# Kernel tuning notes

Measured on AMD Instinct MI355X. Metric: run time of the kernel, lower is better.

## Reference

```python
import jax, jax.numpy as jnp
import numpy as np

H_NODE = 256
H_EDGE = 64
B = 8        # number of graphs
A_PER = 64   # anchors per graph
N_PER = 512  # nodes per graph
INF = 1000000.0
EPS = 1e-8
D_MIN, D_MAX = 0.0, 20.0  # _rbf defaults (gvp-style)


def setup_inputs() -> dict:
    key = jax.random.key(0)
    ks = jax.random.split(key, 16)
    h, he = H_NODE, H_EDGE
    n = lambda k, shp, s=1.0: jax.random.normal(k, shp, jnp.float32) * s
    return {
        "anchor_x": n(ks[0], (B * A_PER, 3), 10.0),
        "node_x": n(ks[1], (B * N_PER, 3), 10.0),
        "anchor_features": n(ks[2], (B * A_PER, h)),
        "node_features": n(ks[3], (B * N_PER, h)),
        "batch": jnp.repeat(jnp.arange(B, dtype=jnp.int32), N_PER),
        "anchor_batch": jnp.repeat(jnp.arange(B, dtype=jnp.int32), A_PER),
        "node_mask": (jax.random.uniform(ks[4], (B * N_PER,)) < 0.9).astype(jnp.float32),
        "Wq": n(ks[5], (h, h), h ** -0.5), "bq": jnp.zeros((h,), jnp.float32),
        "Wkv": n(ks[6], (2 * h, h + he), (h + he) ** -0.5), "bkv": jnp.zeros((2 * h,), jnp.float32),
        "ln1_g": jnp.ones((h,), jnp.float32), "ln1_b": jnp.zeros((h,), jnp.float32),
        "W1": n(ks[7], (2 * h, h), h ** -0.5), "b1": jnp.zeros((2 * h,), jnp.float32),
        "W2": n(ks[8], (2 * h, 2 * h), (2 * h) ** -0.5), "b2": jnp.zeros((2 * h,), jnp.float32),
        "W3": n(ks[9], (h, 2 * h), (2 * h) ** -0.5), "b3": jnp.zeros((h,), jnp.float32),
        "ln2_g": jnp.ones((h,), jnp.float32), "ln2_b": jnp.zeros((h,), jnp.float32),
    }


def _ln(x, g, b, eps=1e-5):
    m = x.mean(-1, keepdims=True)
    v = ((x - m) ** 2).mean(-1, keepdims=True)
    return (x - m) * jax.lax.rsqrt(v + eps) * g + b


def _forward(anchor_x, node_x, anchor_features, node_features, node_mask,
             Wq, bq, Wkv, bkv, ln1_g, ln1_b, W1, b1, W2, b2, W3, b3, ln2_g, ln2_b):
    h, he = H_NODE, H_EDGE
    # equal-sized graphs: reshape global tensors to [B, ., .] (batch ids are repeat(arange(B)))
    q = (anchor_features @ Wq.T + bq).reshape(B, A_PER, h)
    ax = anchor_x.reshape(B, A_PER, 3)
    nx = node_x.reshape(B, N_PER, 3)
    nf = node_features.reshape(B, N_PER, h)
    mask = node_mask.reshape(B, N_PER)

    # pairwise anchor->node distances; original adds scalar eps to the diff vector before the norm
    dist = jnp.linalg.norm(ax[:, :, None, :] - nx[:, None, :, :] + EPS, axis=-1)  # [B,A,N]

    # RBF featurization of dist/10 with D_count = h_edge
    mu = jnp.linspace(D_MIN, D_MAX, he)
    sigma = (D_MAX - D_MIN) / he
    rbf = jnp.exp(-(((dist / 10.0)[..., None] - mu) / sigma) ** 2)  # [B,A,N,he]

    # kv_node(cat([node_feat, rbf])) decomposed: node part computed once per node
    Wkv_n, Wkv_e = Wkv[:, :h], Wkv[:, h:]
    kv_n = nf @ Wkv_n.T + bkv                 # [B,N,2h]
    kv_e = rbf @ Wkv_e.T                      # [B,A,N,2h]
    kv = kv_n[:, None, :, :] + kv_e           # [B,A,N,2h]
    k, v = kv[..., :h], kv[..., h:]

    attn = jnp.einsum('bah,banh->ban', q, k)
    attn = attn * ((mask[:, None, :] - 1.0) * INF)  # faithful to original (multiplicative mask)
    attn = jax.nn.softmax(attn, axis=-1)
    upd = jnp.einsum('ban,banh->bah', attn, v).reshape(B * A_PER, h)

    af = _ln(anchor_features + upd, ln1_g, ln1_b)
    m = jax.nn.relu(af @ W1.T + b1)
    m = jax.nn.relu(m @ W2.T + b2)
    m = m @ W3.T + b3
    return _ln(af + m, ln2_g, ln2_b)


def reference(anchor_x, node_x, anchor_features, node_features, batch, anchor_batch, node_mask,
              Wq, bq, Wkv, bkv, ln1_g, ln1_b, W1, b1, W2, b2, W3, b3, ln2_g, ln2_b):
    # batch / anchor_batch encode equal-sized contiguous graphs; structure is baked into reshapes
    return _forward(anchor_x, node_x, anchor_features, node_features, node_mask,
                    Wq, bq, Wkv, bkv, ln1_g, ln1_b, W1, b1, W2, b2, W3, b3, ln2_g, ln2_b)
```

## Files before the change

kernel.cpp:

```cpp
#include <hip/hip_runtime.h>

#define H    256
#define HE   64
#define NPB  512
#define MU_STEP (20.0f / 63.0f)
#define INV_SIG 3.2f

__device__ __forceinline__ float wave_sum(float v) {
#pragma unroll
    for (int o = 32; o; o >>= 1) v += __shfl_xor(v, o, 64);
    return v;
}
__device__ __forceinline__ float wave_max(float v) {
#pragma unroll
    for (int o = 32; o; o >>= 1) v = fmaxf(v, __shfl_xor(v, o, 64));
    return v;
}
__device__ __forceinline__ float dot4(float4 a, float4 b, float acc) {
    return fmaf(a.x, b.x, fmaf(a.y, b.y, fmaf(a.z, b.z, fmaf(a.w, b.w, acc))));
}
__device__ __forceinline__ float4 add4(float4 a, float4 b) {
    return make_float4(a.x + b.x, a.y + b.y, a.z + b.z, a.w + b.w);
}

__global__ void __launch_bounds__(1024, 4) fused_all(
    const float* __restrict__ anchor_x, const float* __restrict__ node_x,
    const float* __restrict__ anchor_f, const float* __restrict__ node_f,
    const float* __restrict__ node_mask,
    const float* __restrict__ Wq,  const float* __restrict__ bq,
    const float* __restrict__ Wkv, const float* __restrict__ bkv,
    const float* __restrict__ ln1_g, const float* __restrict__ ln1_b,
    const float* __restrict__ W1, const float* __restrict__ b1,
    const float* __restrict__ W2, const float* __restrict__ b2,
    const float* __restrict__ W3, const float* __restrict__ b3,
    const float* __restrict__ g2,  const float* __restrict__ bb2,
    float* __restrict__ out)
{
    const int bid = blockIdx.x;
    const int b  = bid & 7;
    const int pr = bid >> 3;
    const int aA = b * 64 + 2 * pr;
    const int aB = aA + 1;
    const int t  = threadIdx.x;
    const int wv = t >> 6, l = t & 63;
    const int sub = l >> 4, kc16 = l & 15;

    __shared__ __align__(16) float qWp_s[2][2][324];
    __shared__ __align__(16) float q_s[2][256];
    __shared__ __align__(16) float af_s[2][256];
    __shared__ __align__(16) float d10_s[2][NPB];
    __shared__ __align__(16) float mf_s[NPB];
    __shared__ __align__(16) float lg_s[2][NPB];
    __shared__ __align__(16) float w_s[2][NPB];
    __shared__ __align__(16) float snf_s[2][256], rj_s[2][64];
    __shared__ __align__(16) float m1_s[2][512], m2_s[2][512];
    __shared__ __align__(16) float red[512], red16[32];
    __shared__ int   idx_s[2][NPB];
    __shared__ int   cnt_s[2];

    if (t < 128) {
        int hh = t >> 6, tt = t & 63;
        ((float4*)af_s[hh])[tt] =
            ((const float4*)anchor_f)[(size_t)(hh ? aB : aA) * 64 + tt];
    }
    if (t < 2) cnt_s[t] = 0;

    if (t < 512) {
        float axA0 = anchor_x[3 * aA], axA1 = anchor_x[3 * aA + 1], axA2 = anchor_x[3 * aA + 2];
        float axB0 = anchor_x[3 * aB], axB1 = anchor_x[3 * aB + 1], axB2 = anchor_x[3 * aB + 2];
        int ng = b * NPB + t;
        float nx0 = node_x[3 * ng], nx1 = node_x[3 * ng + 1], nx2 = node_x[3 * ng + 2];
        float dx = axA0 - nx0 + 1e-8f, dy = axA1 - nx1 + 1e-8f, dz = axA2 - nx2 + 1e-8f;
        d10_s[0][t] = sqrtf(dx * dx + dy * dy + dz * dz) * 0.1f;
        dx = axB0 - nx0 + 1e-8f; dy = axB1 - nx1 + 1e-8f; dz = axB2 - nx2 + 1e-8f;
        d10_s[1][t] = sqrtf(dx * dx + dy * dy + dz * dz) * 0.1f;
        mf_s[t] = (node_mask[ng] - 1.0f) * 1000000.0f;
    }
    __syncthreads();

    {
        float4 aA4[4], aB4[4];
#pragma unroll
        for (int v = 0; v < 4; ++v) {
            aA4[v] = ((const float4*)af_s[0])[16 * v + kc16];
            aB4[v] = ((const float4*)af_s[1])[16 * v + kc16];
        }
#pragma unroll
        for (int pass = 0; pass < 4; ++pass) {
            int m = pass * 64 + wv * 4 + sub;
            const float4* wr = (const float4*)(Wq + (size_t)m * 256);
            float4 w[4];
#pragma unroll
            for (int v = 0; v < 4; ++v) w[v] = wr[16 * v + kc16];
            float aAc = 0.f, aBc = 0.f;
#pragma unroll
            for (int v = 0; v < 4; ++v) {
                aAc = dot4(w[v], aA4[v], aAc);
                aBc = dot4(w[v], aB4[v], aBc);
            }
#pragma unroll
            for (int o = 8; o >= 1; o >>= 1) {
                aAc += __shfl_xor(aAc, o, 64);
                aBc += __shfl_xor(aBc, o, 64);
            }
            if (kc16 == 0) {
                float bv = bq[m];
                q_s[0][m] = aAc + bv;
                q_s[1][m] = aBc + bv;
            }
        }
    }
    __syncthreads();

    {
        int grp = -1, col = 0;
        if (t < 320)                   { grp = 0; col = t; }
        else if (t >= 512 && t < 832)  { grp = 1; col = t - 512; }
        if (grp >= 0) {
            const int r0 = grp * 128;
            const float* qsA = q_s[0] + r0;
            const float* qsB = q_s[1] + r0;
            float accA = 0.f, accB = 0.f;
            for (int o = 0; o < 128; o += 16) {
                float w16[16];
#pragma unroll
                for (int u = 0; u < 16; ++u) w16[u] = Wkv[(size_t)(r0 + o + u) * 320 + col];
#pragma unroll
                for (int u = 0; u < 16; ++u) {
                    accA = fmaf(w16[u], qsA[o + u], accA);
                    accB = fmaf(w16[u], qsB[o + u], accB);
                }
            }
            qWp_s[grp][0][col] = accA;
            qWp_s[grp][1][col] = accB;
        }
    }
    {
        float p = (t < 512) ? q_s[t >> 8][t & 255] * bkv[t & 255] : 0.f;
        p = wave_sum(p);
        if (l == 0) red16[wv] = p;
    }
    __syncthreads();
    const float qbkA = red16[0] + red16[1] + red16[2] + red16[3];
    const float qbkB = red16[4] + red16[5] + red16[6] + red16[7];

    {
        const int g = sub;
        float4 qA4[4], qB4[4];
#pragma unroll
        for (int v = 0; v < 4; ++v) {
            qA4[v] = add4(((const float4*)qWp_s[0][0])[4 * kc16 + v],
                          ((const float4*)qWp_s[1][0])[4 * kc16 + v]);
            qB4[v] = add4(((const float4*)qWp_s[0][1])[4 * kc16 + v],
                          ((const float4*)qWp_s[1][1])[4 * kc16 + v]);
        }
        const float4 qeA4 = add4(((const float4*)(qWp_s[0][0] + 256))[kc16],
                                 ((const float4*)(qWp_s[1][0] + 256))[kc16]);
        const float4 qeB4 = add4(((const float4*)(qWp_s[0][1] + 256))[kc16],
                                 ((const float4*)(qWp_s[1][1] + 256))[kc16]);
        const float mu0 = (4 * kc16 + 0) * MU_STEP, mu1 = (4 * kc16 + 1) * MU_STEP;
        const float mu2 = (4 * kc16 + 2) * MU_STEP, mu3 = (4 * kc16 + 3) * MU_STEP;
        const float4* nfb = (const float4*)(node_f + (size_t)(b * NPB) * 256);

        float4 f[4], fn[4];
        {
            const size_t r0 = (size_t)(wv * 4 + g) * 64 + 4 * kc16;
#pragma unroll
            for (int v = 0; v < 4; ++v) f[v] = nfb[r0 + v];
        }
        for (int it = 0; it < 8; ++it) {
            const int n = it * 64 + wv * 4 + g;
            if (it < 7) {
                const size_t r1 = (size_t)(n + 64) * 64 + 4 * kc16;
#pragma unroll
                for (int v = 0; v < 4; ++v) fn[v] = nfb[r1 + v];
            }
            float sA = 0.f, sB = 0.f;
#pragma unroll
            for (int v = 0; v < 4; ++v) {
                sA = dot4(f[v], qA4[v], sA);
                sB = dot4(f[v], qB4[v], sB);
            }
            const float dA10 = d10_s[0][n], dB10 = d10_s[1][n];
            float u;
            u = (dA10 - mu0) * INV_SIG; sA = fmaf(qeA4.x, __expf(-u * u), sA);
            u = (dA10 - mu1) * INV_SIG; sA = fmaf(qeA4.y, __expf(-u * u), sA);
            u = (dA10 - mu2) * INV_SIG; sA = fmaf(qeA4.z, __expf(-u * u), sA);
            u = (dA10 - mu3) * INV_SIG; sA = fmaf(qeA4.w, __expf(-u * u), sA);
            u = (dB10 - mu0) * INV_SIG; sB = fmaf(qeB4.x, __expf(-u * u), sB);
            u = (dB10 - mu1) * INV_SIG; sB = fmaf(qeB4.y, __expf(-u * u), sB);
            u = (dB10 - mu2) * INV_SIG; sB = fmaf(qeB4.z, __expf(-u * u), sB);
            u = (dB10 - mu3) * INV_SIG; sB = fmaf(qeB4.w, __expf(-u * u), sB);
#pragma unroll
            for (int o = 8; o >= 1; o >>= 1) {
                sA += __shfl_xor(sA, o, 64);
                sB += __shfl_xor(sB, o, 64);
            }
            if (kc16 == 0) {
                lg_s[0][n] = (sA + qbkA) * mf_s[n];
                lg_s[1][n] = (sB + qbkB) * mf_s[n];
            }
#pragma unroll
            for (int v = 0; v < 4; ++v) f[v] = fn[v];
        }
    }
    __syncthreads();

    const int h8 = t >> 9, n9 = t & 511;
    float lg = lg_s[h8][n9];
    {
        float m = wave_max(lg);
        if (l == 0) red16[wv] = m;
    }
    __syncthreads();
    float gmA = red16[0], gmB = red16[8];
#pragma unroll
    for (int i = 1; i < 8; ++i) { gmA = fmaxf(gmA, red16[i]); gmB = fmaxf(gmB, red16[8 + i]); }
    float e = __expf(lg - (h8 ? gmB : gmA));
    w_s[h8][n9] = e;
    {
        float sm = wave_sum(e);
        if (l == 0) red16[16 + wv] = sm;
    }
    if (e > 0.f) { int p = atomicAdd(&cnt_s[h8], 1); idx_s[h8][p] = n9; }
    __syncthreads();
    float smA = 0.f, smB = 0.f;
#pragma unroll
    for (int i = 0; i < 8; ++i) { smA += red16[16 + i]; smB += red16[24 + i]; }
    const float invA = 1.0f / smA, invB = 1.0f / smB;

    if (t < 512) {
        const int hh = t >> 8, col = t & 255;
        const int cnt = cnt_s[hh];
        const float* base = node_f + (size_t)(b * NPB) * 256 + col;
        const int*   idx  = idx_s[hh];
        const float* ws   = w_s[hh];
        float s = 0.f;
        int i = 0;
        for (; i + 16 <= cnt; i += 16) {
            int   n[16];
            float f[16];
#pragma unroll
            for (int u = 0; u < 16; ++u) n[u] = idx[i + u];
#pragma unroll
            for (int u = 0; u < 16; ++u) f[u] = base[(size_t)n[u] * 256];
#pragma unroll
            for (int u = 0; u < 16; ++u) s = fmaf(ws[n[u]], f[u], s);
        }
        for (; i < cnt; ++i) { int n = idx[i]; s = fmaf(ws[n], base[(size_t)n * 256], s); }
        snf_s[hh][col] = s;
    } else {
        const int tt = t - 512;
        const int ha = tt >> 8, j = tt & 63, g = (tt >> 6) & 3;
        const int cnt = cnt_s[ha];
        const int*   idx = idx_s[ha];
        const float* ws  = w_s[ha];
        const float* ds  = d10_s[ha];
        const float mu = j * MU_STEP;
        float r = 0.f;
        int i = g;
        for (; i + 12 < cnt; i += 16) {
            int n0 = idx[i], n1 = idx[i + 4], n2 = idx[i + 8], n3 = idx[i + 12];
            float u0 = (ds[n0] - mu) * INV_SIG, u1 = (ds[n1] - mu) * INV_SIG;
            float u2 = (ds[n2] - mu) * INV_SIG, u3 = (ds[n3] - mu) * INV_SIG;
            r = fmaf(ws[n0], __expf(-u0 * u0), r);
            r = fmaf(ws[n1], __expf(-u1 * u1), r);
            r = fmaf(ws[n2], __expf(-u2 * u2), r);
            r = fmaf(ws[n3], __expf(-u3 * u3), r);
        }
        for (; i < cnt; i += 4) {
            int n = idx[i];
            float uu = (ds[n] - mu) * INV_SIG;
            r = fmaf(ws[n], __expf(-uu * uu), r);
        }
        red[tt] = r;
    }
    __syncthreads();
    if (t < 128) {
        int ha = t >> 6, j = t & 63;
        rj_s[ha][j] = red[ha * 256 + j] + red[ha * 256 + 64 + j]
                    + red[ha * 256 + 128 + j] + red[ha * 256 + 192 + j];
    }
    __syncthreads();

    {
        float4 sA4[4], sB4[4];
#pragma unroll
        for (int v = 0; v < 4; ++v) {
            sA4[v] = ((const float4*)snf_s[0])[16 * v + kc16];
            sB4[v] = ((const float4*)snf_s[1])[16 * v + kc16];
        }
        const float4 rA4 = ((const float4*)rj_s[0])[kc16];
        const float4 rB4 = ((const float4*)rj_s[1])[kc16];
#pragma unroll
        for (int pass = 0; pass < 4; ++pass) {
            int m = pass * 64 + wv * 4 + sub;
            const float4* wr = (const float4*)(Wkv + (size_t)(256 + m) * 320);
            float4 w[4];
#pragma unroll
            for (int v = 0; v < 4; ++v) w[v] = wr[16 * v + kc16];
            float4 w4 = wr[64 + kc16];
            float aAc = 0.f, aBc = 0.f;
#pragma unroll
            for (int v = 0; v < 4; ++v) {
                aAc = dot4(w[v], sA4[v], aAc);
                aBc = dot4(w[v], sB4[v], aBc);
            }
            aAc = dot4(w4, rA4, aAc);
            aBc = dot4(w4, rB4, aBc);
#pragma unroll
            for (int o = 8; o >= 1; o >>= 1) {
                aAc += __shfl_xor(aAc, o, 64);
                aBc += __shfl_xor(aBc, o, 64);
            }
            if (kc16 == 0) { red[m] = aAc; red[256 + m] = aBc; }
        }
    }
    __syncthreads();

    const int h = (t >> 8) & 1, th = t & 255;
    float x = 0.f;
    if (t < 512)
        x = af_s[h][th] + red[h * 256 + th] * (h ? invB : invA) + bkv[256 + th];
    {
        float s1 = wave_sum(x);
        float s2 = wave_sum(x * x);
        if (l == 0) { red16[wv] = s1; red16[16 + wv] = s2; }
    }
    __syncthreads();
    {
        float meanA = (red16[0] + red16[1] + red16[2] + red16[3]) * (1.0f / 256.0f);
        float meanB = (red16[4] + red16[5] + red16[6] + red16[7]) * (1.0f / 256.0f);
        float sqA   = (red16[16] + red16[17] + red16[18] + red16[19]) * (1.0f / 256.0f);
        float sqB   = (red16[20] + red16[21] + red16[22] + red16[23]) * (1.0f / 256.0f);
        float varA = sqA - meanA * meanA, varB = sqB - meanB * meanB;
        if (t < 512) {
            float xc = x - (h ? meanB : meanA);
            af_s[h][th] = xc * rsqrtf((h ? varB : varA) + 1e-5f) * ln1_g[th] + ln1_b[th];
        }
    }
    __syncthreads();

    {
        float4 aA4[4], aB4[4];
#pragma unroll
        for (int v = 0; v < 4; ++v) {
            aA4[v] = ((const float4*)af_s[0])[16 * v + kc16];
            aB4[v] = ((const float4*)af_s[1])[16 * v + kc16];
        }
#pragma unroll
        for (int pass = 0; pass < 8; ++pass) {
            int m = pass * 64 + wv * 4 + sub;
            const float4* wr = (const float4*)(W1 + (size_t)m * 256);
            float4 w[4];
#pragma unroll
            for (int v = 0; v < 4; ++v) w[v] = wr[16 * v + kc16];
            float aAc = 0.f, aBc = 0.f;
#pragma unroll
            for (int v = 0; v < 4; ++v) {
                aAc = dot4(w[v], aA4[v], aAc);
                aBc = dot4(w[v], aB4[v], aBc);
            }
#pragma unroll
            for (int o = 8; o >= 1; o >>= 1) {
                aAc += __shfl_xor(aAc, o, 64);
                aBc += __shfl_xor(aBc, o, 64);
            }
            if (kc16 == 0) {
                float bv = b1[m];
                m1_s[0][m] = fmaxf(aAc + bv, 0.f);
                m1_s[1][m] = fmaxf(aBc + bv, 0.f);
            }
        }
    }
    __syncthreads();

#pragma unroll
    for (int pass = 0; pass < 8; ++pass) {
        int m = pass * 64 + wv * 4 + sub;
        const float4* wr = (const float4*)(W2 + (size_t)m * 512);
        float4 w[8];
#pragma unroll
        for (int k = 0; k < 8; ++k) w[k] = wr[k * 16 + kc16];
        const float4* mA = (const float4*)m1_s[0];
        const float4* mB = (const float4*)m1_s[1];
        float aAc = 0.f, aBc = 0.f;
#pragma unroll
        for (int k = 0; k < 8; ++k) {
            aAc = dot4(w[k], mA[k * 16 + kc16], aAc);
            aBc = dot4(w[k], mB[k * 16 + kc16], aBc);
        }
#pragma unroll
        for (int o = 8; o >= 1; o >>= 1) {
            aAc += __shfl_xor(aAc, o, 64);
            aBc += __shfl_xor(aBc, o, 64);
        }
        if (kc16 == 0) {
            float bv = b2[m];
            m2_s[0][m] = fmaxf(aAc + bv, 0.f);
            m2_s[1][m] = fmaxf(aBc + bv, 0.f);
        }
    }
    __syncthreads();

#pragma unroll
    for (int pass = 0; pass < 4; ++pass) {
        int m = pass * 64 + wv * 4 + sub;
        const float4* wr = (const float4*)(W3 + (size_t)m * 512);
        float4 w[8];
#pragma unroll
        for (int k = 0; k < 8; ++k) w[k] = wr[k * 16 + kc16];
        const float4* mA = (const float4*)m2_s[0];
        const float4* mB = (const float4*)m2_s[1];
        float aAc = 0.f, aBc = 0.f;
#pragma unroll
        for (int k = 0; k < 8; ++k) {
            aAc = dot4(w[k], mA[k * 16 + kc16], aAc);
            aBc = dot4(w[k], mB[k * 16 + kc16], aBc);
        }
#pragma unroll
        for (int o = 8; o >= 1; o >>= 1) {
            aAc += __shfl_xor(aAc, o, 64);
            aBc += __shfl_xor(aBc, o, 64);
        }
        if (kc16 == 0) {
            float bv = b3[m];
            red[m]       = aAc + bv;
            red[256 + m] = aBc + bv;
        }
    }
    __syncthreads();

    float y = 0.f;
    if (t < 512) y = red[h * 256 + th] + af_s[h][th];
    {
        float s1 = wave_sum(y);
        float s2 = wave_sum(y * y);
        if (l == 0) { red16[wv] = s1; red16[16 + wv] = s2; }
    }
    __syncthreads();
    {
        float mnA = (red16[0] + red16[1] + red16[2] + red16[3]) * (1.0f / 256.0f);
        float mnB = (red16[4] + red16[5] + red16[6] + red16[7]) * (1.0f / 256.0f);
        float sqA = (red16[16] + red16[17] + red16[18] + red16[19]) * (1.0f / 256.0f);
        float sqB = (red16[20] + red16[21] + red16[22] + red16[23]) * (1.0f / 256.0f);
        float vrA = sqA - mnA * mnA, vrB = sqB - mnB * mnB;
        if (t < 512) {
            float yc = y - (h ? mnB : mnA);
            int aOut = h ? aB : aA;
            out[(size_t)aOut * 256 + th] =
                yc * rsqrtf((h ? vrB : vrA) + 1e-5f) * g2[th] + bb2[th];
        }
    }
}

extern "C" void kernel_launch(void* const* d_in, const int* in_sizes, int n_in,
                              void* d_out, int out_size, void* d_ws, size_t ws_size,
                              hipStream_t stream)
{
    const float* anchor_x  = (const float*)d_in[0];
    const float* node_x    = (const float*)d_in[1];
    const float* anchor_f  = (const float*)d_in[2];
    const float* node_f    = (const float*)d_in[3];
    const float* node_mask = (const float*)d_in[6];
    const float* Wq        = (const float*)d_in[7];
    const float* bq        = (const float*)d_in[8];
    const float* Wkv       = (const float*)d_in[9];
    const float* bkv       = (const float*)d_in[10];
    const float* ln1_g     = (const float*)d_in[11];
    const float* ln1_b     = (const float*)d_in[12];
    const float* W1        = (const float*)d_in[13];
    const float* b1        = (const float*)d_in[14];
    const float* W2        = (const float*)d_in[15];
    const float* b2        = (const float*)d_in[16];
    const float* W3        = (const float*)d_in[17];
    const float* b3        = (const float*)d_in[18];
    const float* ln2_g     = (const float*)d_in[19];
    const float* ln2_b     = (const float*)d_in[20];

    fused_all<<<256, 1024, 0, stream>>>(anchor_x, node_x, anchor_f, node_f,
                                        node_mask, Wq, bq, Wkv, bkv,
                                        ln1_g, ln1_b, W1, b1, W2, b2, W3, b3,
                                        ln2_g, ln2_b, (float*)d_out);
}
```

Baseline: 144.7 us.

## Software-pipeline weight loads and replace sparse index gather with dense loops

Adds double-buffered register prefetch of weight rows across passes in the Wq, Wkv, W1, W2 and W3 matvecs, so global loads for the next pass are issued before the current pass's FMAs. It also removes the atomic compaction of nonzero softmax weights into an index list. The node-feature and RBF reductions now loop densely over all 512 nodes with prefetched loads and several independent accumulators. The aim is to hide memory latency and drop the atomic and the indirect gathers. The cost is extra register pressure and about 10% more work on masked nodes whose weight is zero.

```diff
diff --git a/kernel.cpp b/kernel.cpp
--- a/kernel.cpp
+++ b/kernel.cpp
@@ -55,15 +55,12 @@
     __shared__ __align__(16) float snf_s[2][256], rj_s[2][64];
     __shared__ __align__(16) float m1_s[2][512], m2_s[2][512];
     __shared__ __align__(16) float red[512], red16[32];
-    __shared__ int   idx_s[2][NPB];
-    __shared__ int   cnt_s[2];
 
     if (t < 128) {
         int hh = t >> 6, tt = t & 63;
         ((float4*)af_s[hh])[tt] =
             ((const float4*)anchor_f)[(size_t)(hh ? aB : aA) * 64 + tt];
     }
-    if (t < 2) cnt_s[t] = 0;
 
     if (t < 512) {
         float axA0 = anchor_x[3 * aA], axA1 = anchor_x[3 * aA + 1], axA2 = anchor_x[3 * aA + 2];
@@ -85,18 +82,26 @@
             aA4[v] = ((const float4*)af_s[0])[16 * v + kc16];
             aB4[v] = ((const float4*)af_s[1])[16 * v + kc16];
         }
+        float4 w0[4], w1[4];
+        {
+            const float4* wr = (const float4*)(Wq + (size_t)(wv * 4 + sub) * 256);
+#pragma unroll
+            for (int v = 0; v < 4; ++v) w0[v] = wr[16 * v + kc16];
+        }
 #pragma unroll
         for (int pass = 0; pass < 4; ++pass) {
-            int m = pass * 64 + wv * 4 + sub;
-            const float4* wr = (const float4*)(Wq + (size_t)m * 256);
-            float4 w[4];
-#pragma unroll
-            for (int v = 0; v < 4; ++v) w[v] = wr[16 * v + kc16];
+            float4* wc = (pass & 1) ? w1 : w0;
+            float4* wn = (pass & 1) ? w0 : w1;
+            if (pass < 3) {
+                const float4* wr = (const float4*)(Wq + (size_t)((pass + 1) * 64 + wv * 4 + sub) * 256);
+#pragma unroll
+                for (int v = 0; v < 4; ++v) wn[v] = wr[16 * v + kc16];
+            }
             float aAc = 0.f, aBc = 0.f;
 #pragma unroll
             for (int v = 0; v < 4; ++v) {
-                aAc = dot4(w[v], aA4[v], aAc);
-                aBc = dot4(w[v], aB4[v], aBc);
+                aAc = dot4(wc[v], aA4[v], aAc);
+                aBc = dot4(wc[v], aB4[v], aBc);
             }
 #pragma unroll
             for (int o = 8; o >= 1; o >>= 1) {
@@ -104,6 +109,7 @@
                 aBc += __shfl_xor(aBc, o, 64);
             }
             if (kc16 == 0) {
+                int m = pass * 64 + wv * 4 + sub;
                 float bv = bq[m];
                 q_s[0][m] = aAc + bv;
                 q_s[1][m] = aBc + bv;
@@ -121,14 +127,26 @@
             const float* qsA = q_s[0] + r0;
             const float* qsB = q_s[1] + r0;
             float accA = 0.f, accB = 0.f;
-            for (int o = 0; o < 128; o += 16) {
-                float w16[16];
-#pragma unroll
-                for (int u = 0; u < 16; ++u) w16[u] = Wkv[(size_t)(r0 + o + u) * 320 + col];
+            float wb0[16], wb1[16];
+#pragma unroll
+            for (int u = 0; u < 16; ++u) wb0[u] = Wkv[(size_t)(r0 + u) * 320 + col];
+#pragma unroll
+            for (int o = 0; o < 128; o += 32) {
+#pragma unroll
+                for (int u = 0; u < 16; ++u) wb1[u] = Wkv[(size_t)(r0 + o + 16 + u) * 320 + col];
 #pragma unroll
                 for (int u = 0; u < 16; ++u) {
-                    accA = fmaf(w16[u], qsA[o + u], accA);
-                    accB = fmaf(w16[u], qsB[o + u], accB);
+                    accA = fmaf(wb0[u], qsA[o + u], accA);
+                    accB = fmaf(wb0[u], qsB[o + u], accB);
+                }
+                if (o + 32 < 128) {
+#pragma unroll
+                    for (int u = 0; u < 16; ++u) wb0[u] = Wkv[(size_t)(r0 + o + 32 + u) * 320 + col];
+                }
+#pragma unroll
+                for (int u = 0; u < 16; ++u) {
+                    accA = fmaf(wb1[u], qsA[o + 16 + u], accA);
+                    accB = fmaf(wb1[u], qsB[o + 16 + u], accB);
                 }
             }
             qWp_s[grp][0][col] = accA;
@@ -222,7 +240,6 @@
         float sm = wave_sum(e);
         if (l == 0) red16[16 + wv] = sm;
     }
-    if (e > 0.f) { int p = atomicAdd(&cnt_s[h8], 1); idx_s[h8][p] = n9; }
     __syncthreads();
     float smA = 0.f, smB = 0.f;
 #pragma unroll
@@ -231,49 +248,43 @@
 
     if (t < 512) {
         const int hh = t >> 8, col = t & 255;
-        const int cnt = cnt_s[hh];
         const float* base = node_f + (size_t)(b * NPB) * 256 + col;
-        const int*   idx  = idx_s[hh];
         const float* ws   = w_s[hh];
         float s = 0.f;
-        int i = 0;
-        for (; i + 16 <= cnt; i += 16) {
-            int   n[16];
-            float f[16];
-#pragma unroll
-            for (int u = 0; u < 16; ++u) n[u] = idx[i + u];
-#pragma unroll
-            for (int u = 0; u < 16; ++u) f[u] = base[(size_t)n[u] * 256];
-#pragma unroll
-            for (int u = 0; u < 16; ++u) s = fmaf(ws[n[u]], f[u], s);
-        }
-        for (; i < cnt; ++i) { int n = idx[i]; s = fmaf(ws[n], base[(size_t)n * 256], s); }
+        float f0[8], f1[8];
+#pragma unroll
+        for (int u = 0; u < 8; ++u) f0[u] = base[(size_t)u * 256];
+        for (int i = 0; i < 512; i += 16) {
+#pragma unroll
+            for (int u = 0; u < 8; ++u) f1[u] = base[(size_t)(i + 8 + u) * 256];
+#pragma unroll
+            for (int u = 0; u < 8; ++u) s = fmaf(ws[i + u], f0[u], s);
+            if (i + 16 < 512) {
+#pragma unroll
+                for (int u = 0; u < 8; ++u) f0[u] = base[(size_t)(i + 16 + u) * 256];
+            }
+#pragma unroll
+            for (int u = 0; u < 8; ++u) s = fmaf(ws[i + 8 + u], f1[u], s);
+        }
         snf_s[hh][col] = s;
     } else {
         const int tt = t - 512;
-        const int ha = tt >> 8, j = tt & 63, g = (tt >> 6) & 3;
-        const int cnt = cnt_s[ha];
-        const int*   idx = idx_s[ha];
-        const float* ws  = w_s[ha];
-        const float* ds  = d10_s[ha];
+        const int ha = tt >> 8, j = tt & 63, g4 = (tt >> 6) & 3;
+        const float* ws = w_s[ha];
+        const float* ds = d10_s[ha];
         const float mu = j * MU_STEP;
-        float r = 0.f;
-        int i = g;
-        for (; i + 12 < cnt; i += 16) {
-            int n0 = idx[i], n1 = idx[i + 4], n2 = idx[i + 8], n3 = idx[i + 12];
-            float u0 = (ds[n0] - mu) * INV_SIG, u1 = (ds[n1] - mu) * INV_SIG;
-            float u2 = (ds[n2] - mu) * INV_SIG, u3 = (ds[n3] - mu) * INV_SIG;
-            r = fmaf(ws[n0], __expf(-u0 * u0), r);
-            r = fmaf(ws[n1], __expf(-u1 * u1), r);
-            r = fmaf(ws[n2], __expf(-u2 * u2), r);
-            r = fmaf(ws[n3], __expf(-u3 * u3), r);
-        }
-        for (; i < cnt; i += 4) {
-            int n = idx[i];
-            float uu = (ds[n] - mu) * INV_SIG;
-            r = fmaf(ws[n], __expf(-uu * uu), r);
-        }
-        red[tt] = r;
+        float r0 = 0.f, r1 = 0.f, r2 = 0.f, r3 = 0.f;
+        for (int i = g4; i < 512; i += 16) {
+            float u0 = (ds[i]      - mu) * INV_SIG;
+            float u1 = (ds[i + 4]  - mu) * INV_SIG;
+            float u2 = (ds[i + 8]  - mu) * INV_SIG;
+            float u3 = (ds[i + 12] - mu) * INV_SIG;
+            r0 = fmaf(ws[i],      __expf(-u0 * u0), r0);
+            r1 = fmaf(ws[i + 4],  __expf(-u1 * u1), r1);
+            r2 = fmaf(ws[i + 8],  __expf(-u2 * u2), r2);
+            r3 = fmaf(ws[i + 12], __expf(-u3 * u3), r3);
+        }
+        red[tt] = (r0 + r1) + (r2 + r3);
     }
     __syncthreads();
     if (t < 128) {
@@ -292,28 +303,41 @@
         }
         const float4 rA4 = ((const float4*)rj_s[0])[kc16];
         const float4 rB4 = ((const float4*)rj_s[1])[kc16];
+        float4 w0[4], w1[4], w40, w41;
+        {
+            const float4* wr = (const float4*)(Wkv + (size_t)(256 + wv * 4 + sub) * 320);
+#pragma unroll
+            for (int v = 0; v < 4; ++v) w0[v] = wr[16 * v + kc16];
+            w40 = wr[64 + kc16];
+        }
 #pragma unroll
         for (int pass = 0; pass < 4; ++pass) {
-            int m = pass * 64 + wv * 4 + sub;
-            const float4* wr = (const float4*)(Wkv + (size_t)(256 + m) * 320);
-            float4 w[4];
-#pragma unroll
-            for (int v = 0; v < 4; ++v) w[v] = wr[16 * v + kc16];
-            float4 w4 = wr[64 + kc16];
+            float4* wc = (pass & 1) ? w1 : w0;
+            float4* wn = (pass & 1) ? w0 : w1;
+            float4  w4c = (pass & 1) ? w41 : w40;
+            if (pass < 3) {
+                const float4* wr = (const float4*)(Wkv + (size_t)(256 + (pass + 1) * 64 + wv * 4 + sub) * 320);
+#pragma unroll
+                for (int v = 0; v < 4; ++v) wn[v] = wr[16 * v + kc16];
+                if (pass & 1) w40 = wr[64 + kc16]; else w41 = wr[64 + kc16];
+            }
             float aAc = 0.f, aBc = 0.f;
 #pragma unroll
             for (int v = 0; v < 4; ++v) {
-                aAc = dot4(w[v], sA4[v], aAc);
-                aBc = dot4(w[v], sB4[v], aBc);
-            }
-            aAc = dot4(w4, rA4, aAc);
-            aBc = dot4(w4, rB4, aBc);
+                aAc = dot4(wc[v], sA4[v], aAc);
+                aBc = dot4(wc[v], sB4[v], aBc);
+            }
+            aAc = dot4(w4c, rA4, aAc);
+            aBc = dot4(w4c, rB4, aBc);
 #pragma unroll
             for (int o = 8; o >= 1; o >>= 1) {
                 aAc += __shfl_xor(aAc, o, 64);
                 aBc += __shfl_xor(aBc, o, 64);
             }
-            if (kc16 == 0) { red[m] = aAc; red[256 + m] = aBc; }
+            if (kc16 == 0) {
+                int m = pass * 64 + wv * 4 + sub;
+                red[m] = aAc; red[256 + m] = aBc;
+            }
         }
     }
     __syncthreads();
@@ -348,18 +372,26 @@
             aA4[v] = ((const float4*)af_s[0])[16 * v + kc16];
             aB4[v] = ((const float4*)af_s[1])[16 * v + kc16];
         }
+        float4 w0[4], w1[4];
+        {
+            const float4* wr = (const float4*)(W1 + (size_t)(wv * 4 + sub) * 256);
+#pragma unroll
+            for (int v = 0; v < 4; ++v) w0[v] = wr[16 * v + kc16];
+        }
 #pragma unroll
         for (int pass = 0; pass < 8; ++pass) {
-            int m = pass * 64 + wv * 4 + sub;
-            const float4* wr = (const float4*)(W1 + (size_t)m * 256);
-            float4 w[4];
-#pragma unroll
-            for (int v = 0; v < 4; ++v) w[v] = wr[16 * v + kc16];
+            float4* wc = (pass & 1) ? w1 : w0;
+            float4* wn = (pass & 1) ? w0 : w1;
+            if (pass < 7) {
+                const float4* wr = (const float4*)(W1 + (size_t)((pass + 1) * 64 + wv * 4 + sub) * 256);
+#pragma unroll
+                for (int v = 0; v < 4; ++v) wn[v] = wr[16 * v + kc16];
+            }
             float aAc = 0.f, aBc = 0.f;
 #pragma unroll
             for (int v = 0; v < 4; ++v) {
-                aAc = dot4(w[v], aA4[v], aAc);
-                aBc = dot4(w[v], aB4[v], aBc);
+                aAc = dot4(wc[v], aA4[v], aAc);
+                aBc = dot4(wc[v], aB4[v], aBc);
             }
 #pragma unroll
             for (int o = 8; o >= 1; o >>= 1) {
@@ -367,6 +399,7 @@
                 aBc += __shfl_xor(aBc, o, 64);
             }
             if (kc16 == 0) {
+                int m = pass * 64 + wv * 4 + sub;
                 float bv = b1[m];
                 m1_s[0][m] = fmaxf(aAc + bv, 0.f);
                 m1_s[1][m] = fmaxf(aBc + bv, 0.f);
@@ -375,58 +408,92 @@
     }
     __syncthreads();
 
-#pragma unroll
-    for (int pass = 0; pass < 8; ++pass) {
-        int m = pass * 64 + wv * 4 + sub;
-        const float4* wr = (const float4*)(W2 + (size_t)m * 512);
-        float4 w[8];
-#pragma unroll
-        for (int k = 0; k < 8; ++k) w[k] = wr[k * 16 + kc16];
+    {
         const float4* mA = (const float4*)m1_s[0];
         const float4* mB = (const float4*)m1_s[1];
-        float aAc = 0.f, aBc = 0.f;
-#pragma unroll
-        for (int k = 0; k < 8; ++k) {
-            aAc = dot4(w[k], mA[k * 16 + kc16], aAc);
-            aBc = dot4(w[k], mB[k * 16 + kc16], aBc);
-        }
-#pragma unroll
-        for (int o = 8; o >= 1; o >>= 1) {
-            aAc += __shfl_xor(aAc, o, 64);
-            aBc += __shfl_xor(aBc, o, 64);
-        }
-        if (kc16 == 0) {
-            float bv = b2[m];
-            m2_s[0][m] = fmaxf(aAc + bv, 0.f);
-            m2_s[1][m] = fmaxf(aBc + bv, 0.f);
-        }
-    }
-    __syncthreads();
-
-#pragma unroll
-    for (int pass = 0; pass < 4; ++pass) {
-        int m = pass * 64 + wv * 4 + sub;
-        const float4* wr = (const float4*)(W3 + (size_t)m * 512);
-        float4 w[8];
-#pragma unroll
-        for (int k = 0; k < 8; ++k) w[k] = wr[k * 16 + kc16];
+        float4 w0[4], w1[4];
+        {
+            const float4* wr = (const float4*)(W2 + (size_t)(wv * 4 + sub) * 512);
+#pragma unroll
+            for (int v = 0; v < 4; ++v) w0[v] = wr[v * 16 + kc16];
+        }
+#pragma unroll
+        for (int pass = 0; pass < 8; ++pass) {
+            int m = pass * 64 + wv * 4 + sub;
+            const float4* wr = (const float4*)(W2 + (size_t)m * 512);
+            float aAc = 0.f, aBc = 0.f;
+#pragma unroll
+            for (int v = 0; v < 4; ++v) w1[v] = wr[(4 + v) * 16 + kc16];
+#pragma unroll
+            for (int v = 0; v < 4; ++v) {
+                aAc = dot4(w0[v], mA[v * 16 + kc16], aAc);
+                aBc = dot4(w0[v], mB[v * 16 + kc16], aBc);
+            }
+            if (pass < 7) {
+                const float4* wrn = (const float4*)(W2 + (size_t)(m + 64) * 512);
+#pragma unroll
+                for (int v = 0; v < 4; ++v) w0[v] = wrn[v * 16 + kc16];
+            }
+#pragma unroll
+            for (int v = 0; v < 4; ++v) {
+                aAc = dot4(w1[v], mA[(4 + v) * 16 + kc16], aAc);
+                aBc = dot4(w1[v], mB[(4 + v) * 16 + kc16], aBc);
+            }
+#pragma unroll
+            for (int o = 8; o >= 1; o >>= 1) {
+                aAc += __shfl_xor(aAc, o, 64);
+                aBc += __shfl_xor(aBc, o, 64);
+            }
+            if (kc16 == 0) {
+                float bv = b2[m];
+                m2_s[0][m] = fmaxf(aAc + bv, 0.f);
+                m2_s[1][m] = fmaxf(aBc + bv, 0.f);
+            }
+        }
+    }
+    __syncthreads();
+
+    {
         const float4* mA = (const float4*)m2_s[0];
         const float4* mB = (const float4*)m2_s[1];
-        float aAc = 0.f, aBc = 0.f;
-#pragma unroll
-        for (int k = 0; k < 8; ++k) {
-            aAc = dot4(w[k], mA[k * 16 + kc16], aAc);
-            aBc = dot4(w[k], mB[k * 16 + kc16], aBc);
-        }
-#pragma unroll
-        for (int o = 8; o >= 1; o >>= 1) {
-            aAc += __shfl_xor(aAc, o, 64);
-            aBc += __shfl_xor(aBc, o, 64);
-        }
-        if (kc16 == 0) {
-            float bv = b3[m];
-            red[m]       = aAc + bv;
-            red[256 + m] = aBc + bv;
+        float4 w0[4], w1[4];
+        {
+            const float4* wr = (const float4*)(W3 + (size_t)(wv * 4 + sub) * 512);
+#pragma unroll
+            for (int v = 0; v < 4; ++v) w0[v] = wr[v * 16 + kc16];
+        }
+#pragma unroll
+        for (int pass = 0; pass < 4; ++pass) {
+            int m = pass * 64 + wv * 4 + sub;
+            const float4* wr = (const float4*)(W3 + (size_t)m * 512);
+            float aAc = 0.f, aBc = 0.f;
+#pragma unroll
+            for (int v = 0; v < 4; ++v) w1[v] = wr[(4 + v) * 16 + kc16];
+#pragma unroll
+            for (int v = 0; v < 4; ++v) {
+                aAc = dot4(w0[v], mA[v * 16 + kc16], aAc);
+                aBc = dot4(w0[v], mB[v * 16 + kc16], aBc);
+            }
+            if (pass < 3) {
+                const float4* wrn = (const float4*)(W3 + (size_t)(m + 64) * 512);
+#pragma unroll
+                for (int v = 0; v < 4; ++v) w0[v] = wrn[v * 16 + kc16];
+            }
+#pragma unroll
+            for (int v = 0; v < 4; ++v) {
+                aAc = dot4(w1[v], mA[(4 + v) * 16 + kc16], aAc);
+                aBc = dot4(w1[v], mB[(4 + v) * 16 + kc16], aBc);
+            }
+#pragma unroll
+            for (int o = 8; o >= 1; o >>= 1) {
+                aAc += __shfl_xor(aAc, o, 64);
+                aBc += __shfl_xor(aBc, o, 64);
+            }
+            if (kc16 == 0) {
+                float bv = b3[m];
+                red[m]       = aAc + bv;
+                red[256 + m] = aBc + bv;
+            }
         }
     }
     __syncthreads();
```

Result: slower. 153.3 us (+5.9%).
